# Performance work log

Hardware: AMD Instinct MI355X
Metric: run time of the kernel (lower is better)

The kernel has to match this reference:

```python
import jax, jax.numpy as jnp
import numpy as np

HEAD_SIZE = 64

def setup_inputs() -> dict:
    key = jax.random.key(0)
    k1, k2, k3, k4 = jax.random.split(key, 4)
    B, T, C = 4, 4096, 768
    s = 1.0 / np.sqrt(C)
    return {
        "x": jax.random.normal(k1, (B, T, C), dtype=jnp.float32),
        "Wq": jax.random.normal(k2, (C, HEAD_SIZE), dtype=jnp.float32) * s,
        "Wk": jax.random.normal(k3, (C, HEAD_SIZE), dtype=jnp.float32) * s,
        "Wv": jax.random.normal(k4, (C, HEAD_SIZE), dtype=jnp.float32) * s,
    }

def reference(x, Wq, Wk, Wv):
    # x: [B,T,C]; Wq/Wk/Wv: [C,H]
    T = x.shape[1]
    q = jnp.einsum('btc,ch->bth', x, Wq)
    k = jnp.einsum('btc,ch->bth', x, Wk)
    v = jnp.einsum('btc,ch->bth', x, Wv)
    scale = HEAD_SIZE ** (-0.5)
    wei = jnp.einsum('bth,bsh->bts', q, k) * scale  # [B,T,T]
    causal = jnp.tril(jnp.ones((T, T), dtype=bool))
    wei = jnp.where(causal, wei, -jnp.inf)
    wei = jax.nn.softmax(wei, axis=-1)
    # dropout p=0.0 -> identity
    out = jnp.einsum('bts,bsh->bth', wei, v)  # [B,T,H]
    return out
```

## Files before the change

### kernel.cpp

```cpp
#include <hip/hip_runtime.h>
#include <hip/hip_bf16.h>
#include <stdint.h>
#include <math.h>

typedef unsigned short u16;
typedef __attribute__((ext_vector_type(8))) __bf16 bf16x8;
typedef __attribute__((ext_vector_type(4))) float f32x4;

#define LOG2E 1.44269504088896340736f

__device__ inline u16 f2bf(float f){
  uint32_t u = __float_as_uint(f);
  u += 0x7FFFu + ((u >> 16) & 1u);
  return (u16)(u >> 16);
}
__device__ inline float bf2f(u16 v){
  return __uint_as_float(((uint32_t)v) << 16);
}

__global__ __launch_bounds__(256) void wt_kernel(const float* __restrict__ Wq,
                                                 const float* __restrict__ Wk,
                                                 const float* __restrict__ Wv,
                                                 u16* __restrict__ wtf){
  int idx = blockIdx.x * 256 + threadIdx.x;
  if (idx >= 192 * 768) return;
  int n = idx / 768, c = idx - n * 768;
  int h = n & 63;
  const float* W = (n < 64) ? Wq : ((n < 128) ? Wk : Wv);
  float v = W[c * 64 + h];
  if (n < 64) v *= 0.125f * LOG2E;
  int f = n >> 4, n16 = n & 15;
  int kstep = c >> 5, quad = (c >> 3) & 3, j = c & 7;
  wtf[(size_t)((f * 24 + kstep) * 64 + quad * 16 + n16) * 8 + j] = f2bf(v);
}

__global__ __launch_bounds__(256) void proj_kernel(const float* __restrict__ x,
                                                   const u16* __restrict__ wtf,
                                                   u16* __restrict__ qs,
                                                   u16* __restrict__ ksf,
                                                   u16* __restrict__ vtf){
  __shared__ u16 At[24 * 64 * 8];
  const int tid = threadIdx.x;
  const int w = tid >> 6, lane = tid & 63;
  const int n16 = lane & 15, quad = lane >> 4;
  const int rt = blockIdx.x * 16;

  const float* xb = x + (size_t)rt * 768;
  float4 t[12];
#pragma unroll
  for (int i = 0; i < 12; ++i)
    t[i] = *(const float4*)(xb + (size_t)(i * 256 + tid) * 4);
#pragma unroll
  for (int i = 0; i < 12; ++i){
    int l = i * 256 + tid;
    int row = l / 192, c4 = l - row * 192;
    int ksn = c4 >> 3, qd = (c4 >> 1) & 3, j0 = (c4 & 1) * 4;
    int idx = ((ksn * 64 + qd * 16 + row) * 8 + j0) ^ ((ksn & 7) << 3);
    union { ushort4 s; u16 e[4]; } pk;
    pk.e[0] = f2bf(t[i].x); pk.e[1] = f2bf(t[i].y);
    pk.e[2] = f2bf(t[i].z); pk.e[3] = f2bf(t[i].w);
    *(ushort4*)&At[idx] = pk.s;
  }
  __syncthreads();

  const f32x4 fz = {0.f, 0.f, 0.f, 0.f};
  f32x4 acc[3];
#pragma unroll
  for (int j = 0; j < 3; ++j) acc[j] = fz;

#pragma unroll
  for (int kst = 0; kst < 24; ++kst){
    const int sw = (kst & 7) << 3;
    bf16x8 a = *(const bf16x8*)&At[((kst * 64 + lane) * 8) ^ sw];
#pragma unroll
    for (int j = 0; j < 3; ++j){
      bf16x8 bfr = *(const bf16x8*)(wtf + (size_t)(((3 * w + j) * 24 + kst) * 64 + lane) * 8);
      acc[j] = __builtin_amdgcn_mfma_f32_16x16x32_bf16(a, bfr, acc[j], 0, 0, 0);
    }
  }
  __syncthreads();

#pragma unroll
  for (int j = 0; j < 3; ++j){
    const int F = 3 * w + j;
    const int s = F >> 2, c0 = (F & 3) * 16;
#pragma unroll
    for (int r = 0; r < 4; ++r){
      u16 val = f2bf(acc[j][r]);
      int row = quad * 4 + r;
      if (s < 2) At[s * 1152 + row * 72 + c0 + n16] = val;
      else       At[2304 + (c0 + n16) * 24 + row]   = val;
    }
  }
  __syncthreads();

  const int bb = rt >> 12, t0 = rt & 4095;
  const int kt = t0 >> 6;
  const int fk = (t0 >> 4) & 3;
  const int half0 = (t0 >> 5) & 1;
  const int qhalf = (t0 >> 4) & 1;
  if (tid < 128){
    int row = tid >> 3, hc = tid & 7;
    uint4 qv = *(const uint4*)&At[row * 72 + hc * 8];
    *(uint4*)(qs + (size_t)(rt + row) * 64 + hc * 8) = qv;
  } else {
    int tt = tid - 128;
    int half = tt >> 6, l2 = tt & 63;
    int nn = l2 & 15, qq = l2 >> 4;
    uint4 kv = *(const uint4*)&At[1152 + nn * 72 + half * 32 + qq * 8];
    size_t off = ((((size_t)(bb * 64 + kt) * 4 + fk) * 2 + half) * 64 + l2) * 8;
    *(uint4*)(ksf + off) = kv;
  }
  if (tid < 128){
    int f = tid >> 5, idx5 = tid & 31;
    int qsel = idx5 >> 4, nn = idx5 & 15;
    int h = f * 16 + nn;
    uint4 vv = *(const uint4*)&At[2304 + h * 24 + qsel * 8];
    int lane2 = (2 * qhalf + qsel) * 16 + nn;
    size_t off = ((((size_t)(bb * 64 + kt) * 4 + f) * 2 + half0) * 64 + lane2) * 8;
    *(uint4*)(vtf + off) = vv;
  }
}

__global__ __launch_bounds__(256) void flash_part(const u16* __restrict__ qs,
                                                  const u16* __restrict__ ksf,
                                                  const u16* __restrict__ vtf,
                                                  u16* __restrict__ Opart,
                                                  float* __restrict__ ml){
  const int gid = blockIdx.x;
  int b, qt, ck, nt;
  if (gid < 1024){
    b = gid >> 8;
    int r = gid & 255;
    int m = (int)sqrtf((float)r);
    if (m * m > r) --m;
    if ((m + 1) * (m + 1) <= r) ++m;
    int d = r - m * m;
    if (d < m){ qt = 2 * m;     ck = d;     }
    else      { qt = 2 * m + 1; ck = d - m; }
    nt = 4;
  } else {
    int t = gid - 1024;
    b = t >> 4;
    int m = t & 15;
    qt = 2 * m; ck = m; nt = 2;
  }
  const int kt0 = ck * 4;

  __shared__ u16 Kb[4096];
  __shared__ u16 Vb[4096];
  __shared__ u16 Ps[128 * 72];
  const int tid = threadIdx.x;
  const int w = tid >> 6, lane = tid & 63;
  const int n16 = lane & 15, quad = lane >> 4;

  const u16* qb  = qs  + (size_t)b * 262144;
  const u16* kpg = ksf + (size_t)b * 262144 + (size_t)kt0 * 4096;
  const u16* vpg = vtf + (size_t)b * 262144 + (size_t)kt0 * 4096;

  bf16x8 qA[2][2];
#pragma unroll
  for (int m = 0; m < 2; ++m){
    const size_t qrow = (size_t)(qt * 128 + w * 32 + m * 16 + n16) * 64;
    qA[m][0] = *(const bf16x8*)(qb + qrow + quad * 8);
    qA[m][1] = *(const bf16x8*)(qb + qrow + 32 + quad * 8);
  }

  const f32x4 fz = {0.f, 0.f, 0.f, 0.f};
  f32x4 O[2][4];
  float rs[2][4];
#pragma unroll
  for (int m = 0; m < 2; ++m)
#pragma unroll
    for (int f = 0; f < 4; ++f){ O[m][f] = fz; rs[m][f] = 0.f; }

  uint4 rk0, rk1, rv0, rv1;
#define LOADR(ti)                                                            \
  {                                                                          \
    const u16* kg = kpg + (size_t)(ti) * 4096 + tid * 16;                    \
    const u16* vg = vpg + (size_t)(ti) * 4096 + tid * 16;                    \
    rk0 = *(const uint4*)kg;  rk1 = *(const uint4*)(kg + 8);                 \
    rv0 = *(const uint4*)vg;  rv1 = *(const uint4*)(vg + 8);                 \
  }
#define WRITES()                                                             \
  {                                                                          \
    *(uint4*)&Kb[tid * 16] = rk0;  *(uint4*)&Kb[tid * 16 + 8] = rk1;         \
    *(uint4*)&Vb[tid * 16] = rv0;  *(uint4*)&Vb[tid * 16 + 8] = rv1;         \
  }

  LOADR(0);
  WRITES();
  if (nt > 1) LOADR(1);
  __syncthreads();

  for (int it = 0; it < nt; ++it){
    const int kt = kt0 + it;

    f32x4 S[2][4];
#pragma unroll
    for (int f = 0; f < 4; ++f){
      bf16x8 k0 = *(const bf16x8*)&Kb[(f * 2 + 0) * 512 + lane * 8];
      bf16x8 k1 = *(const bf16x8*)&Kb[(f * 2 + 1) * 512 + lane * 8];
#pragma unroll
      for (int m = 0; m < 2; ++m){
        f32x4 s = fz;
        s = __builtin_amdgcn_mfma_f32_16x16x32_bf16(qA[m][0], k0, s, 0, 0, 0);
        s = __builtin_amdgcn_mfma_f32_16x16x32_bf16(qA[m][1], k1, s, 0, 0, 0);
        S[m][f] = s;
      }
    }

    if (kt >= 2 * qt){
#pragma unroll
      for (int m = 0; m < 2; ++m)
#pragma unroll
        for (int f = 0; f < 4; ++f)
#pragma unroll
          for (int r = 0; r < 4; ++r){
            int col = kt * 64 + f * 16 + n16;
            int row = qt * 128 + w * 32 + m * 16 + quad * 4 + r;
            if (col > row) S[m][f][r] = -1e30f;
          }
    }

#pragma unroll
    for (int m = 0; m < 2; ++m)
#pragma unroll
      for (int f = 0; f < 4; ++f)
#pragma unroll
        for (int r = 0; r < 4; ++r){
          float p = __builtin_amdgcn_exp2f(S[m][f][r]);
          S[m][f][r] = p;
          rs[m][r] += p;
        }

#pragma unroll
    for (int m = 0; m < 2; ++m)
#pragma unroll
      for (int f = 0; f < 4; ++f){
        u16* p = &Ps[(w * 32 + m * 16 + quad * 4) * 72 + f * 16 + n16];
        p[0]   = f2bf(S[m][f][0]);
        p[72]  = f2bf(S[m][f][1]);
        p[144] = f2bf(S[m][f][2]);
        p[216] = f2bf(S[m][f][3]);
      }
    bf16x8 pA[2][2];
#pragma unroll
    for (int m = 0; m < 2; ++m){
      pA[m][0] = *(const bf16x8*)&Ps[(w * 32 + m * 16 + n16) * 72 + quad * 8];
      pA[m][1] = *(const bf16x8*)&Ps[(w * 32 + m * 16 + n16) * 72 + 32 + quad * 8];
    }

#pragma unroll
    for (int f = 0; f < 4; ++f){
      bf16x8 v0 = *(const bf16x8*)&Vb[(f * 2 + 0) * 512 + lane * 8];
      bf16x8 v1 = *(const bf16x8*)&Vb[(f * 2 + 1) * 512 + lane * 8];
#pragma unroll
      for (int m = 0; m < 2; ++m){
        O[m][f] = __builtin_amdgcn_mfma_f32_16x16x32_bf16(pA[m][0], v0, O[m][f], 0, 0, 0);
        O[m][f] = __builtin_amdgcn_mfma_f32_16x16x32_bf16(pA[m][1], v1, O[m][f], 0, 0, 0);
      }
    }

    if (it + 1 < nt){
      __syncthreads();
      WRITES();
      if (it + 2 < nt) LOADR(it + 2);
      __syncthreads();
    }
  }
#undef LOADR
#undef WRITES

#pragma unroll
  for (int m = 0; m < 2; ++m)
#pragma unroll
    for (int r = 0; r < 4; ++r){
#pragma unroll
      for (int off = 1; off < 16; off <<= 1)
        rs[m][r] += __shfl_xor(rs[m][r], off, 16);
    }

  const size_t oidx = (size_t)gid * 8192;
#pragma unroll
  for (int m = 0; m < 2; ++m)
#pragma unroll
    for (int f = 0; f < 4; ++f)
#pragma unroll
      for (int r = 0; r < 4; ++r){
        int row_local = w * 32 + m * 16 + quad * 4 + r;
        Opart[oidx + (size_t)row_local * 64 + f * 16 + n16] = f2bf(O[m][f][r]);
      }
  if (n16 == 0){
    float* lp = ml + (size_t)gid * 128;
#pragma unroll
    for (int m = 0; m < 2; ++m)
#pragma unroll
      for (int r = 0; r < 4; ++r)
        lp[w * 32 + m * 16 + quad * 4 + r] = rs[m][r];
  }
}

__global__ __launch_bounds__(256) void combine_kernel(const u16* __restrict__ Opart,
                                                      const float* __restrict__ ml,
                                                      float* __restrict__ out){
  const int gid = blockIdx.x * 256 + threadIdx.x;
  const int bq = gid >> 11;
  const int rem = (gid & 2047) * 4;
  const int row = rem >> 6;
  const int b = bq >> 5, qt = bq & 31;
  const int m = qt >> 1;
  const int nc4 = (qt & 1) ? (m + 1) : m;
  const int F = (qt & 1) ? (m * m + m) : (m * m);

  float L = 0.f;
  float a0 = 0.f, a1 = 0.f, a2 = 0.f, a3 = 0.f;
  for (int j = 0; j < nc4; ++j){
    int p = b * 256 + F + j;
    L += ml[(size_t)p * 128 + row];
    const u16* q = Opart + (size_t)p * 8192 + rem;
    uint2 d = *(const uint2*)q;
    a0 += bf2f((u16)(d.x & 0xffffu));
    a1 += bf2f((u16)(d.x >> 16));
    a2 += bf2f((u16)(d.y & 0xffffu));
    a3 += bf2f((u16)(d.y >> 16));
  }
  if (!(qt & 1)){
    int p = 1024 + b * 16 + m;
    L += ml[(size_t)p * 128 + row];
    const u16* q = Opart + (size_t)p * 8192 + rem;
    uint2 d = *(const uint2*)q;
    a0 += bf2f((u16)(d.x & 0xffffu));
    a1 += bf2f((u16)(d.x >> 16));
    a2 += bf2f((u16)(d.y & 0xffffu));
    a3 += bf2f((u16)(d.y >> 16));
  }
  const float invL = 1.0f / L;
  float4 v = {a0 * invL, a1 * invL, a2 * invL, a3 * invL};
  *(float4*)(out + (size_t)gid * 4) = v;
}

extern "C" void kernel_launch(void* const* d_in, const int* in_sizes, int n_in,
                              void* d_out, int out_size, void* d_ws, size_t ws_size,
                              hipStream_t stream){
  const float* x  = (const float*)d_in[0];
  const float* Wq = (const float*)d_in[1];
  const float* Wk = (const float*)d_in[2];
  const float* Wv = (const float*)d_in[3];
  float* out = (float*)d_out;

  u16* qs  = (u16*)d_ws;
  u16* ksf = qs  + (size_t)16384 * 64;
  u16* vtf = ksf + (size_t)16384 * 64;
  u16* wtf = vtf + (size_t)16384 * 64;
  u16* Opart = wtf + (size_t)192 * 768;
  float* ml = (float*)(Opart + (size_t)1088 * 8192);

  wt_kernel<<<576, 256, 0, stream>>>(Wq, Wk, Wv, wtf);
  proj_kernel<<<1024, 256, 0, stream>>>(x, wtf, qs, ksf, vtf);
  flash_part<<<1088, 256, 0, stream>>>(qs, ksf, vtf, Opart, ml);
  combine_kernel<<<1024, 256, 0, stream>>>(Opart, ml, out);
}
```

Measured before the change: 129.2 us.

## Pipeline x loads in projection over K chunks and reorder attention K/V prefetch

The projection kernel now splits the 768-wide reduction into four 192-column chunks, loading the next chunk into registers while MFMAs run on the current one, starting at a per-block rotated chunk. This cuts register pressure (3 float4 instead of 12) and overlaps global loads with compute. In the attention kernel the prefetch of the next K/V tile moves to the start of each iteration instead of after the LDS write, which shortens how long the loads are in flight before use. It also adds extra barriers in the projection kernel.

```diff
diff --git a/kernel.cpp b/kernel.cpp
--- a/kernel.cpp
+++ b/kernel.cpp
@@ -44,41 +44,67 @@
   const int w = tid >> 6, lane = tid & 63;
   const int n16 = lane & 15, quad = lane >> 4;
   const int rt = blockIdx.x * 16;
-
   const float* xb = x + (size_t)rt * 768;
-  float4 t[12];
-#pragma unroll
-  for (int i = 0; i < 12; ++i)
-    t[i] = *(const float4*)(xb + (size_t)(i * 256 + tid) * 4);
-#pragma unroll
-  for (int i = 0; i < 12; ++i){
-    int l = i * 256 + tid;
-    int row = l / 192, c4 = l - row * 192;
-    int ksn = c4 >> 3, qd = (c4 >> 1) & 3, j0 = (c4 & 1) * 4;
-    int idx = ((ksn * 64 + qd * 16 + row) * 8 + j0) ^ ((ksn & 7) << 3);
-    union { ushort4 s; u16 e[4]; } pk;
-    pk.e[0] = f2bf(t[i].x); pk.e[1] = f2bf(t[i].y);
-    pk.e[2] = f2bf(t[i].z); pk.e[3] = f2bf(t[i].w);
-    *(ushort4*)&At[idx] = pk.s;
-  }
-  __syncthreads();
+
+  float4 tr0, tr1, tr2;
+#define LOADR(c) {                                                           \
+    int jj0 = tid,       r0 = jj0 / 48, q0 = jj0 - r0 * 48;                  \
+    int jj1 = 256 + tid, r1 = jj1 / 48, q1 = jj1 - r1 * 48;                  \
+    int jj2 = 512 + tid, r2 = jj2 / 48, q2 = jj2 - r2 * 48;                  \
+    tr0 = *(const float4*)(xb + ((size_t)r0 * 192 + (c) * 48 + q0) * 4);     \
+    tr1 = *(const float4*)(xb + ((size_t)r1 * 192 + (c) * 48 + q1) * 4);     \
+    tr2 = *(const float4*)(xb + ((size_t)r2 * 192 + (c) * 48 + q2) * 4);     \
+  }
+#define WR1(c, jj, t) {                                                      \
+    int rr = (jj) / 48, ql = (jj) - rr * 48;                                 \
+    int ksn = (c) * 6 + (ql >> 3), qd = (ql >> 1) & 3, j0 = (ql & 1) * 4;    \
+    int idx = ((ksn * 64 + qd * 16 + rr) * 8 + j0) ^ ((ksn & 7) << 3);       \
+    union { ushort4 s; u16 e[4]; } pk;                                       \
+    pk.e[0] = f2bf(t.x); pk.e[1] = f2bf(t.y);                                \
+    pk.e[2] = f2bf(t.z); pk.e[3] = f2bf(t.w);                                \
+    *(ushort4*)&At[idx] = pk.s;                                              \
+  }
+#define WRITES(c) { WR1(c, tid, tr0); WR1(c, 256 + tid, tr1); WR1(c, 512 + tid, tr2); }
+#define COMPUTE(c) {                                                         \
+    _Pragma("unroll") for (int kk = 0; kk < 6; ++kk){                        \
+      int kst = (c) * 6 + kk;                                                \
+      int sw = (kst & 7) << 3;                                               \
+      bf16x8 a = *(const bf16x8*)&At[((kst * 64 + lane) * 8) ^ sw];          \
+      _Pragma("unroll") for (int j = 0; j < 3; ++j){                         \
+        bf16x8 bfr = *(const bf16x8*)(wtf + (size_t)(((3 * w + j) * 24 + kst) * 64 + lane) * 8); \
+        acc[j] = __builtin_amdgcn_mfma_f32_16x16x32_bf16(a, bfr, acc[j], 0, 0, 0); \
+      }                                                                      \
+    }                                                                        \
+  }
 
   const f32x4 fz = {0.f, 0.f, 0.f, 0.f};
   f32x4 acc[3];
 #pragma unroll
   for (int j = 0; j < 3; ++j) acc[j] = fz;
 
-#pragma unroll
-  for (int kst = 0; kst < 24; ++kst){
-    const int sw = (kst & 7) << 3;
-    bf16x8 a = *(const bf16x8*)&At[((kst * 64 + lane) * 8) ^ sw];
-#pragma unroll
-    for (int j = 0; j < 3; ++j){
-      bf16x8 bfr = *(const bf16x8*)(wtf + (size_t)(((3 * w + j) * 24 + kst) * 64 + lane) * 8);
-      acc[j] = __builtin_amdgcn_mfma_f32_16x16x32_bf16(a, bfr, acc[j], 0, 0, 0);
-    }
-  }
-  __syncthreads();
+  const int ch0 = blockIdx.x & 3;
+  const int ch1 = (ch0 + 1) & 3, ch2 = (ch0 + 2) & 3, ch3 = (ch0 + 3) & 3;
+
+  LOADR(ch0); WRITES(ch0);
+  __syncthreads();
+  LOADR(ch1);
+  COMPUTE(ch0);
+  WRITES(ch1);
+  __syncthreads();
+  LOADR(ch2);
+  COMPUTE(ch1);
+  WRITES(ch2);
+  __syncthreads();
+  LOADR(ch3);
+  COMPUTE(ch2);
+  WRITES(ch3);
+  __syncthreads();
+  COMPUTE(ch3);
+  __syncthreads();
+#undef LOADR
+#undef WR1
+#undef WRITES
+#undef COMPUTE
 
 #pragma unroll
   for (int j = 0; j < 3; ++j){
@@ -190,11 +216,11 @@
 
   LOADR(0);
   WRITES();
-  if (nt > 1) LOADR(1);
   __syncthreads();
 
   for (int it = 0; it < nt; ++it){
     const int kt = kt0 + it;
+    if (it + 1 < nt) LOADR(it + 1);
 
     f32x4 S[2][4];
 #pragma unroll
@@ -265,7 +291,6 @@
     if (it + 1 < nt){
       __syncthreads();
       WRITES();
-      if (it + 2 < nt) LOADR(it + 2);
       __syncthreads();
     }
   }
```

Result: no change. 128.9 us (-0.2%).
